# Kernel optimization log

Hardware: AMD Instinct MI355X
Metric: run time of the kernel (lower is better)

Reference implementation:

```python
import jax, jax.numpy as jnp
import numpy as np

B, S, E, N, H = 2, 2048, 2048, 16, 128  # batch, seq, embed, heads, depth


def sine_table(features, length, min_timescale=1.0, max_timescale=10000.0):
    fraction = jnp.arange(0, features, 2, dtype=jnp.float32) / features
    timescale = min_timescale * (max_timescale / min_timescale) ** fraction
    sinusoid_inp = jnp.einsum('i,j->ij', jnp.arange(length, dtype=jnp.float32), 1.0 / timescale,
                              precision=jax.lax.Precision.HIGHEST)
    sinusoid_inp = jnp.concatenate([sinusoid_inp, sinusoid_inp], axis=-1)  # [L, features]
    return jnp.sin(sinusoid_inp), jnp.cos(sinusoid_inp)


def rotate_half(x):
    x1, x2 = jnp.split(x, 2, axis=-1)
    return jnp.concatenate([-x2, x1], axis=-1)


def apply_rotary(q, k, cos, sin):
    # q: [B,S,N,H], k: [B,T,N,H]; cos/sin: [L,H] broadcast over (seq, depth)
    qcos = cos[: q.shape[1]][None, :, None, :]
    qsin = sin[: q.shape[1]][None, :, None, :]
    kcos = cos[: k.shape[1]][None, :, None, :]
    ksin = sin[: k.shape[1]][None, :, None, :]
    return q * qcos + rotate_half(q) * qsin, k * kcos + rotate_half(k) * ksin


def setup_inputs() -> dict:
    key = jax.random.key(0)
    ks = jax.random.split(key, 6)
    scale = 1.0 / np.sqrt(E)
    return {
        'x_q': jax.random.normal(ks[0], (B, S, E), jnp.float32),
        'x_kv': jax.random.normal(ks[1], (B, S, E), jnp.float32),
        'WQ': jax.random.normal(ks[2], (E, N, H), jnp.float32) * scale,
        'WK': jax.random.normal(ks[3], (E, N, H), jnp.float32) * scale,
        'WV': jax.random.normal(ks[4], (E, N, H), jnp.float32) * scale,
        'WO': jax.random.normal(ks[5], (N, H, E), jnp.float32) * scale,
    }


def reference(x_q, x_kv, WQ, WK, WV, WO):
    q = jnp.einsum('bse,enh->bsnh', x_q, WQ)
    k = jnp.einsum('bte,enh->btnh', x_kv, WK)
    v = jnp.einsum('bte,enh->btnh', x_kv, WV)

    sin, cos = sine_table(q.shape[-1], max(q.shape[1], k.shape[1]))
    q, k = apply_rotary(q, k, cos, sin)

    # causal attention bias: [1,1,S,T]
    s_len, t_len = q.shape[1], k.shape[1]
    causal = jnp.arange(s_len)[:, None] >= jnp.arange(t_len)[None, :]
    bias = jnp.where(causal, 0.0, -1e10).astype(jnp.float32)[None, None]

    logits = jnp.einsum('bsnh,btnh->bnst', q, k) / np.sqrt(H) + bias
    probs = jax.nn.softmax(logits, axis=-1)
    a = jnp.einsum('bnst,btnh->bsnh', probs, v)
    o = jnp.einsum('bsnh,nhe->bse', a, WO)
    return o
```

## Files before the change

kernel.cpp:

```cpp
#include <hip/hip_runtime.h>
#include <hip/hip_bf16.h>

typedef __bf16 bf16;
typedef __attribute__((ext_vector_type(8))) __bf16 bf16x8;
typedef __attribute__((ext_vector_type(4))) __bf16 bf16x4;
typedef __attribute__((ext_vector_type(4))) float f32x4;

typedef const __attribute__((address_space(1))) void* gptr_t;
typedef __attribute__((address_space(3))) void* sptr_t;

__device__ __forceinline__ void gload16(const void* g, void* l) {
  __builtin_amdgcn_global_load_lds((gptr_t)g, (sptr_t)l, 16, 0, 0);
}

#define MFMA_BF16(a, b, c) __builtin_amdgcn_mfma_f32_16x16x32_bf16((a), (b), (c), 0, 0, 0)

namespace {
constexpr int kB = 2, kS = 2048, kE = 2048, kN = 16, kH = 128;
constexpr int kBS = kB * kS;
constexpr int kNH = kN * kH;
constexpr float kScale = 0.08838834764831845f;
constexpr float kLog2e = 1.4426950408889634f;
}

__global__ void k_cvt(const float* __restrict__ in, bf16* __restrict__ out) {
  int i = blockIdx.x * 256 + threadIdx.x;
  float4 v = reinterpret_cast<const float4*>(in)[i];
  bf16x4 o = { (bf16)v.x, (bf16)v.y, (bf16)v.z, (bf16)v.w };
  reinterpret_cast<bf16x4*>(out)[i] = o;
}

__global__ void k_tconv(const float* __restrict__ in, bf16* __restrict__ out) {
  __shared__ bf16 tile[64][66];
  int bx = blockIdx.x & 31, by = blockIdx.x >> 5;
  int r0 = by * 64, c0 = bx * 64;
  int t = threadIdx.x;
  int c = t & 63, rb = t >> 6;
#pragma unroll
  for (int j = 0; j < 16; ++j) {
    int r = rb + j * 4;
    tile[r][c] = (bf16)in[(size_t)(r0 + r) * 2048 + c0 + c];
  }
  __syncthreads();
  int rr = t & 63;
#pragma unroll
  for (int j = 0; j < 16; ++j) {
    int cc = rb + j * 4;
    out[(size_t)(c0 + cc) * 2048 + r0 + rr] = tile[rr][cc];
  }
}

__global__ void k_vtrans(const bf16* __restrict__ V, bf16* __restrict__ Vt) {
  __shared__ bf16 tile[64][66];
  int bid = blockIdx.x;
  int bn = bid >> 6;
  int s0 = ((bid >> 1) & 31) * 64;
  int h0 = (bid & 1) * 64;
  size_t base = (size_t)bn * kS * kH;
  int t = threadIdx.x, c = t & 63, rb = t >> 6;
#pragma unroll
  for (int j = 0; j < 16; ++j) {
    int r = rb + j * 4;
    tile[r][c] = V[base + (size_t)(s0 + r) * kH + h0 + c];
  }
  __syncthreads();
#pragma unroll
  for (int j = 0; j < 16; ++j) {
    int hh = rb + j * 4;
    Vt[base + (size_t)(h0 + hh) * kS + s0 + (t & 63)] = tile[t & 63][hh];
  }
}

__global__ void k_rope(bf16* __restrict__ Qd, bf16* __restrict__ Kd) {
  int tid = blockIdx.x * 256 + threadIdx.x;
  int i = tid & 63;
  int s = (tid >> 6) & (kS - 1);
  int bn = tid >> 17;
  size_t base = ((size_t)bn * kS + s) * kH;
  float inv = exp2f(-(float)i * 0.20762050593046457f);
  float ang = (float)s * inv;
  float sn, cs;
  sincosf(ang, &sn, &cs);
  float q1 = (float)Qd[base + i], q2 = (float)Qd[base + i + 64];
  Qd[base + i]      = (bf16)(q1 * cs - q2 * sn);
  Qd[base + i + 64] = (bf16)(q2 * cs + q1 * sn);
  float k1 = (float)Kd[base + i], k2 = (float)Kd[base + i + 64];
  Kd[base + i]      = (bf16)(k1 * cs - k2 * sn);
  Kd[base + i + 64] = (bf16)(k2 * cs + k1 * sn);
}

template <int MODE>
__global__ __launch_bounds__(256, 2) void k_gemm(const bf16* __restrict__ A,
                                                 const bf16* __restrict__ Bt,
                                                 void* __restrict__ Cout) {
  constexpr int Kk = 2048;
  __shared__ __align__(16) bf16 As[128][32];
  __shared__ __align__(16) bf16 Bs[128][32];
  int bid = blockIdx.x;
  int swz = (bid & 7) * 64 + (bid >> 3);
  int mt = swz >> 4, nt = swz & 15;
  int m0 = mt * 128, n0 = nt * 128;
  int t = threadIdx.x, wid = t >> 6, lane = t & 63;
  int l16 = lane & 15, lq = lane >> 4;
  int wr = wid >> 1, wc = wid & 1;
  f32x4 acc[4][4] = {};

  for (int kt = 0; kt < Kk / 32; ++kt) {
    int k0 = kt * 32;
#pragma unroll
    for (int i = 0; i < 2; ++i) {
      int idx = i * 256 + t;
      const bf16* ga = A + (size_t)(m0 + (idx >> 2)) * Kk + k0 + (idx & 3) * 8;
      gload16(ga, (char*)(&As[0][0]) + i * 4096 + wid * 1024);
      const bf16* gb = Bt + (size_t)(n0 + (idx >> 2)) * Kk + k0 + (idx & 3) * 8;
      gload16(gb, (char*)(&Bs[0][0]) + i * 4096 + wid * 1024);
    }
    __syncthreads();
    bf16x8 af[4], bfr[4];
#pragma unroll
    for (int mi = 0; mi < 4; ++mi)
      af[mi] = *(const bf16x8*)&As[wr * 64 + mi * 16 + l16][lq * 8];
#pragma unroll
    for (int ni = 0; ni < 4; ++ni)
      bfr[ni] = *(const bf16x8*)&Bs[wc * 64 + ni * 16 + l16][lq * 8];
#pragma unroll
    for (int mi = 0; mi < 4; ++mi)
#pragma unroll
      for (int ni = 0; ni < 4; ++ni)
        acc[mi][ni] = MFMA_BF16(af[mi], bfr[ni], acc[mi][ni]);
    __syncthreads();
  }

#pragma unroll
  for (int mi = 0; mi < 4; ++mi) {
    int mrow_base = m0 + wr * 64 + mi * 16 + lq * 4;
#pragma unroll
    for (int ni = 0; ni < 4; ++ni) {
      int col = n0 + wc * 64 + ni * 16 + l16;
#pragma unroll
      for (int r = 0; r < 4; ++r) {
        int mrow = mrow_base + r;
        float v = acc[mi][ni][r];
        if (MODE == 0) {
          int b = mrow >> 11, s = mrow & 2047, n = col >> 7, h = col & 127;
          ((bf16*)Cout)[(((size_t)(b * kN + n) * kS + s)) * kH + h] = (bf16)v;
        } else {
          ((float*)Cout)[(size_t)mrow * 2048 + col] = v;
        }
      }
    }
  }
}

__global__ __launch_bounds__(512, 4) void k_attn(const bf16* __restrict__ Q,
                                                 const bf16* __restrict__ Kg,
                                                 const bf16* __restrict__ Vt,
                                                 bf16* __restrict__ AO) {
  __shared__ __align__(16) bf16 Ks[64 * 128];
  __shared__ __align__(16) bf16 Vs[128 * 64];
  __shared__ __align__(16) bf16 Ps[8][16][72];
  int bid = blockIdx.x;
  int half = bid >> 8;
  int bn = (half << 4) | ((bid >> 4) & 15);
  int qt = (bid & 15) ^ (half ? 15 : 0);
  int q0 = qt * 128;
  int t = threadIdx.x, wid = t >> 6, lane = t & 63;
  int l16 = lane & 15, lq = lane >> 4;
  size_t bnSH = (size_t)bn * kS * kH;

  int qrow_a = q0 + wid * 16 + l16;
  bf16x8 qf[4];
#pragma unroll
  for (int ks = 0; ks < 4; ++ks)
    qf[ks] = *(const bf16x8*)(Q + bnSH + (size_t)qrow_a * kH + ks * 32 + lq * 8);

  f32x4 oacc[8] = {};
  float mrun[4], lrun[4];
#pragma unroll
  for (int r = 0; r < 4; ++r) { mrun[r] = -1e30f; lrun[r] = 0.f; }

  int ntiles = (q0 + 128) >> 6;
  for (int kt = 0; kt < ntiles; ++kt) {
    int kv0 = kt * 64;
#pragma unroll
    for (int i = 0; i < 2; ++i) {
      int idx = i * 512 + t;
      {
        int row = idx >> 4, ch = idx & 15;
        int gch = ch ^ (row & 7);
        gload16(Kg + bnSH + (size_t)(kv0 + row) * kH + gch * 8,
                (char*)Ks + i * 8192 + wid * 1024);
      }
      {
        int row = idx >> 3, ch = idx & 7;
        int gch = ch ^ (row & 7);
        gload16(Vt + bnSH + (size_t)row * kS + kv0 + gch * 8,
                (char*)Vs + i * 8192 + wid * 1024);
      }
    }
    __syncthreads();

    f32x4 sacc[4] = {};
#pragma unroll
    for (int ks = 0; ks < 4; ++ks) {
#pragma unroll
      for (int ni = 0; ni < 4; ++ni) {
        int sp = ni * 16 + l16;
        int hb = (ks * 32 + lq * 8) * 2;
        bf16x8 kb = *(const bf16x8*)((const char*)Ks + sp * 256 + (hb ^ ((sp & 7) << 4)));
        sacc[ni] = MFMA_BF16(qf[ks], kb, sacc[ni]);
      }
    }

    bool need_mask = (kv0 + 63) > (q0 + wid * 16);
#pragma unroll
    for (int ni = 0; ni < 4; ++ni) {
      f32x4 v = sacc[ni] * kScale;
      if (need_mask) {
#pragma unroll
        for (int r = 0; r < 4; ++r) {
          int qrow = q0 + wid * 16 + lq * 4 + r;
          int col = kv0 + ni * 16 + l16;
          if (col > qrow) v[r] = -1e30f;
        }
      }
      sacc[ni] = v;
    }

#pragma unroll
    for (int r = 0; r < 4; ++r) {
      float pm = fmaxf(fmaxf(sacc[0][r], sacc[1][r]),
                       fmaxf(sacc[2][r], sacc[3][r]));
      pm = fmaxf(pm, __shfl_xor(pm, 1));
      pm = fmaxf(pm, __shfl_xor(pm, 2));
      pm = fmaxf(pm, __shfl_xor(pm, 4));
      pm = fmaxf(pm, __shfl_xor(pm, 8));
      float mold = mrun[r];
      float mnew = fmaxf(mold, pm);
      float alpha = exp2f((mold - mnew) * kLog2e);
      mrun[r] = mnew;
      float rs = 0.f;
#pragma unroll
      for (int ni = 0; ni < 4; ++ni) {
        float p = exp2f((sacc[ni][r] - mnew) * kLog2e);
        sacc[ni][r] = p;
        rs += p;
      }
      rs += __shfl_xor(rs, 1);
      rs += __shfl_xor(rs, 2);
      rs += __shfl_xor(rs, 4);
      rs += __shfl_xor(rs, 8);
      lrun[r] = lrun[r] * alpha + rs;
#pragma unroll
      for (int nj = 0; nj < 8; ++nj) oacc[nj][r] *= alpha;
    }

#pragma unroll
    for (int ni = 0; ni < 4; ++ni)
#pragma unroll
      for (int r = 0; r < 4; ++r)
        Ps[wid][lq * 4 + r][ni * 16 + l16] = (bf16)sacc[ni][r];

#pragma unroll
    for (int ks = 0; ks < 2; ++ks) {
      bf16x8 pa = *(const bf16x8*)&Ps[wid][l16][ks * 32 + lq * 8];
#pragma unroll
      for (int nj = 0; nj < 8; ++nj) {
        int h = nj * 16 + l16;
        int sb = (ks * 64 + lq * 16) ^ ((h & 7) << 4);
        bf16x8 vb = *(const bf16x8*)((const char*)Vs + h * 128 + sb);
        oacc[nj] = MFMA_BF16(pa, vb, oacc[nj]);
      }
    }
    __syncthreads();
  }

  int b = bn >> 4, n = bn & 15;
#pragma unroll
  for (int r = 0; r < 4; ++r) {
    float inv = 1.0f / lrun[r];
    int qrow = q0 + wid * 16 + lq * 4 + r;
#pragma unroll
    for (int nj = 0; nj < 8; ++nj) {
      float v = oacc[nj][r] * inv;
      AO[(((size_t)b * kS + qrow) * kN + n) * kH + nj * 16 + l16] = (bf16)v;
    }
  }
}

extern "C" void kernel_launch(void* const* d_in, const int* in_sizes, int n_in,
                              void* d_out, int out_size, void* d_ws, size_t ws_size,
                              hipStream_t stream) {
  (void)in_sizes; (void)n_in; (void)out_size; (void)ws_size;
  const float* x_q  = (const float*)d_in[0];
  const float* x_kv = (const float*)d_in[1];
  const float* WQ   = (const float*)d_in[2];
  const float* WK   = (const float*)d_in[3];
  const float* WV   = (const float*)d_in[4];
  const float* WO   = (const float*)d_in[5];
  float* out = (float*)d_out;
  char* w = (char*)d_ws;
  const size_t MB = 1ull << 20;
  bf16* xq  = (bf16*)(w + 0 * MB);
  bf16* xkv = (bf16*)(w + 16 * MB);
  bf16* WqT = (bf16*)(w + 32 * MB);
  bf16* WkT = (bf16*)(w + 40 * MB);
  bf16* WvT = (bf16*)(w + 48 * MB);
  bf16* WoT = (bf16*)(w + 56 * MB);
  bf16* Qb  = (bf16*)(w + 64 * MB);
  bf16* Kb  = (bf16*)(w + 80 * MB);
  bf16* Vb  = (bf16*)(w + 96 * MB);
  bf16* AO  = xq;
  bf16* Vtb = xkv;

  k_cvt<<<8192, 256, 0, stream>>>(x_q, xq);
  k_cvt<<<8192, 256, 0, stream>>>(x_kv, xkv);
  k_tconv<<<1024, 256, 0, stream>>>(WQ, WqT);
  k_tconv<<<1024, 256, 0, stream>>>(WK, WkT);
  k_tconv<<<1024, 256, 0, stream>>>(WV, WvT);
  k_tconv<<<1024, 256, 0, stream>>>(WO, WoT);
  k_gemm<0><<<512, 256, 0, stream>>>(xq,  WqT, Qb);
  k_gemm<0><<<512, 256, 0, stream>>>(xkv, WkT, Kb);
  k_gemm<0><<<512, 256, 0, stream>>>(xkv, WvT, Vb);
  k_rope<<<16384, 256, 0, stream>>>(Qb, Kb);
  k_vtrans<<<2048, 256, 0, stream>>>(Vb, Vtb);
  k_attn<<<512, 512, 0, stream>>>(Qb, Kb, Vtb, AO);
  k_gemm<1><<<512, 256, 0, stream>>>(AO, WoT, out);
}
```

Before: 471.5 us.

## Fuse QKV projections into one 256x256 double-buffered pipelined GEMM kernel

Replaces the 128x128 single-buffered GEMM with a 256x256-tile, 512-thread kernel. It uses double-buffered LDS staged through direct global-to-LDS loads, an XOR-swizzled layout, and raised wave priority around the MFMA bursts. The three Q/K/V projections are merged into one launch over the concatenated weight matrix, with each output routed to Q, K or V by column group. The aim is to cut load stalls, barrier overhead and launch count. The larger tiles leave the output projection with only 128 blocks, which underfills the CUs.

```diff
diff --git a/kernel.cpp b/kernel.cpp
--- a/kernel.cpp
+++ b/kernel.cpp
@@ -15,10 +15,10 @@
 
 #define MFMA_BF16(a, b, c) __builtin_amdgcn_mfma_f32_16x16x32_bf16((a), (b), (c), 0, 0, 0)
 
+#define BAR() do { asm volatile("" ::: "memory"); __builtin_amdgcn_s_barrier(); asm volatile("" ::: "memory"); } while (0)
+
 namespace {
 constexpr int kB = 2, kS = 2048, kE = 2048, kN = 16, kH = 128;
-constexpr int kBS = kB * kS;
-constexpr int kNH = kN * kH;
 constexpr float kScale = 0.08838834764831845f;
 constexpr float kLog2e = 1.4426950408889634f;
 }
@@ -89,63 +89,150 @@
   Kd[base + i + 64] = (bf16)(k2 * cs + k1 * sn);
 }
 
+
+__device__ __forceinline__ void stage_half(const bf16* __restrict__ src, size_t row0,
+                                           int k0, char* slot, int t) {
+#pragma unroll
+  for (int i = 0; i < 2; ++i) {
+    int idx = i * 512 + t;
+    int d = idx * 16;
+    int lb = d ^ (((d >> 9) & 1) << 5);
+    int r = lb >> 7;
+    int kc = (lb & 127) >> 1;
+    gload16(src + (row0 + r) * 2048 + k0 + kc,
+            slot + i * 8192 + (t >> 6) * 1024);
+  }
+}
+
 template <int MODE>
-__global__ __launch_bounds__(256, 2) void k_gemm(const bf16* __restrict__ A,
-                                                 const bf16* __restrict__ Bt,
-                                                 void* __restrict__ Cout) {
-  constexpr int Kk = 2048;
-  __shared__ __align__(16) bf16 As[128][32];
-  __shared__ __align__(16) bf16 Bs[128][32];
+__global__ __launch_bounds__(512, 2) void k_gemm8(const bf16* __restrict__ Aq,
+                                                  const bf16* __restrict__ Akv,
+                                                  const bf16* __restrict__ Bt,
+                                                  void* __restrict__ Cout) {
+  constexpr int NTN = (MODE == 0) ? 24 : 8;
+  constexpr int NT = 32;
+  __shared__ __align__(16) char AsB[2][2][16384];
+  __shared__ __align__(16) char BsB[2][2][16384];
   int bid = blockIdx.x;
-  int swz = (bid & 7) * 64 + (bid >> 3);
-  int mt = swz >> 4, nt = swz & 15;
-  int m0 = mt * 128, n0 = nt * 128;
+  constexpr int nblk = 16 * NTN;
+  int swz = (bid & 7) * (nblk >> 3) + (bid >> 3);
+  int mt = swz / NTN, nt = swz - mt * NTN;
+  size_t m0 = (size_t)mt * 256;
+  int n0 = nt * 256;
+  const bf16* A = (MODE == 0 && nt >= 8) ? Akv : Aq;
   int t = threadIdx.x, wid = t >> 6, lane = t & 63;
   int l16 = lane & 15, lq = lane >> 4;
-  int wr = wid >> 1, wc = wid & 1;
-  f32x4 acc[4][4] = {};
-
-  for (int kt = 0; kt < Kk / 32; ++kt) {
-    int k0 = kt * 32;
-#pragma unroll
-    for (int i = 0; i < 2; ++i) {
-      int idx = i * 256 + t;
-      const bf16* ga = A + (size_t)(m0 + (idx >> 2)) * Kk + k0 + (idx & 3) * 8;
-      gload16(ga, (char*)(&As[0][0]) + i * 4096 + wid * 1024);
-      const bf16* gb = Bt + (size_t)(n0 + (idx >> 2)) * Kk + k0 + (idx & 3) * 8;
-      gload16(gb, (char*)(&Bs[0][0]) + i * 4096 + wid * 1024);
-    }
-    __syncthreads();
-    bf16x8 af[4], bfr[4];
-#pragma unroll
-    for (int mi = 0; mi < 4; ++mi)
-      af[mi] = *(const bf16x8*)&As[wr * 64 + mi * 16 + l16][lq * 8];
-#pragma unroll
-    for (int ni = 0; ni < 4; ++ni)
-      bfr[ni] = *(const bf16x8*)&Bs[wc * 64 + ni * 16 + l16][lq * 8];
-#pragma unroll
-    for (int mi = 0; mi < 4; ++mi)
-#pragma unroll
-      for (int ni = 0; ni < 4; ++ni)
-        acc[mi][ni] = MFMA_BF16(af[mi], bfr[ni], acc[mi][ni]);
-    __syncthreads();
-  }
-
-#pragma unroll
-  for (int mi = 0; mi < 4; ++mi) {
-    int mrow_base = m0 + wr * 64 + mi * 16 + lq * 4;
-#pragma unroll
-    for (int ni = 0; ni < 4; ++ni) {
-      int col = n0 + wc * 64 + ni * 16 + l16;
+  int wr = wid >> 2, wc = wid & 3;
+  int bhalf = wc >> 1;
+  int brow0 = ((wc & 1) << 6) + l16;
+
+  f32x4 acc[8][4] = {};
+  bf16x8 af[4], bf[4];
+
+  stage_half(Bt, (size_t)n0,       0, BsB[0][0], t);
+  stage_half(Bt, (size_t)n0 + 128, 0, BsB[0][1], t);
+  stage_half(A,  m0,               0, AsB[0][0], t);
+  stage_half(A,  m0 + 128,         0, AsB[0][1], t);
+  stage_half(Bt, (size_t)n0,      64, BsB[1][0], t);
+  stage_half(Bt, (size_t)n0 + 128, 64, BsB[1][1], t);
+  asm volatile("s_waitcnt vmcnt(4)" ::: "memory");
+  BAR();
+
+  for (int kt = 0; kt < NT; ++kt) {
+    int buf = kt & 1, nbuf = buf ^ 1;
+#pragma unroll
+    for (int j = 0; j < 4; ++j) {
+      int l = ((j * 16 + l16) << 7) + (lq << 4);
+      af[j] = *(const bf16x8*)(AsB[buf][wr] + (l ^ (((l >> 9) & 1) << 5)));
+    }
+#pragma unroll
+    for (int nf = 0; nf < 4; ++nf) {
+      int l = ((brow0 + nf * 16) << 7) + (lq << 4);
+      bf[nf] = *(const bf16x8*)(BsB[buf][bhalf] + (l ^ (((l >> 9) & 1) << 5)));
+    }
+    if (kt + 1 < NT) stage_half(A, m0, (kt + 1) * 64, AsB[nbuf][0], t);
+    BAR();
+    __builtin_amdgcn_s_setprio(1);
+#pragma unroll
+    for (int j = 0; j < 4; ++j)
+#pragma unroll
+      for (int nf = 0; nf < 4; ++nf)
+        acc[j][nf] = MFMA_BF16(af[j], bf[nf], acc[j][nf]);
+    __builtin_amdgcn_s_setprio(0);
+    BAR();
+#pragma unroll
+    for (int j = 0; j < 4; ++j) {
+      int l = (((j + 4) * 16 + l16) << 7) + (lq << 4);
+      af[j] = *(const bf16x8*)(AsB[buf][wr] + (l ^ (((l >> 9) & 1) << 5)));
+    }
+    if (kt + 1 < NT) stage_half(A, m0 + 128, (kt + 1) * 64, AsB[nbuf][1], t);
+    BAR();
+    __builtin_amdgcn_s_setprio(1);
+#pragma unroll
+    for (int j = 0; j < 4; ++j)
+#pragma unroll
+      for (int nf = 0; nf < 4; ++nf)
+        acc[j + 4][nf] = MFMA_BF16(af[j], bf[nf], acc[j + 4][nf]);
+    __builtin_amdgcn_s_setprio(0);
+    BAR();
+#pragma unroll
+    for (int j = 0; j < 4; ++j) {
+      int l = ((j * 16 + l16) << 7) + 64 + (lq << 4);
+      af[j] = *(const bf16x8*)(AsB[buf][wr] + (l ^ (((l >> 9) & 1) << 5)));
+    }
+#pragma unroll
+    for (int nf = 0; nf < 4; ++nf) {
+      int l = ((brow0 + nf * 16) << 7) + 64 + (lq << 4);
+      bf[nf] = *(const bf16x8*)(BsB[buf][bhalf] + (l ^ (((l >> 9) & 1) << 5)));
+    }
+    BAR();
+    __builtin_amdgcn_s_setprio(1);
+#pragma unroll
+    for (int j = 0; j < 4; ++j)
+#pragma unroll
+      for (int nf = 0; nf < 4; ++nf)
+        acc[j][nf] = MFMA_BF16(af[j], bf[nf], acc[j][nf]);
+    __builtin_amdgcn_s_setprio(0);
+    BAR();
+#pragma unroll
+    for (int j = 0; j < 4; ++j) {
+      int l = (((j + 4) * 16 + l16) << 7) + 64 + (lq << 4);
+      af[j] = *(const bf16x8*)(AsB[buf][wr] + (l ^ (((l >> 9) & 1) << 5)));
+    }
+    if (kt + 2 < NT) {
+      stage_half(Bt, (size_t)n0,       (kt + 2) * 64, BsB[buf][0], t);
+      stage_half(Bt, (size_t)n0 + 128, (kt + 2) * 64, BsB[buf][1], t);
+    }
+    BAR();
+    __builtin_amdgcn_s_setprio(1);
+#pragma unroll
+    for (int j = 0; j < 4; ++j)
+#pragma unroll
+      for (int nf = 0; nf < 4; ++nf)
+        acc[j + 4][nf] = MFMA_BF16(af[j], bf[nf], acc[j + 4][nf]);
+    __builtin_amdgcn_s_setprio(0);
+    if (kt < NT - 2)       asm volatile("s_waitcnt vmcnt(4)" ::: "memory");
+    else if (kt == NT - 2) asm volatile("s_waitcnt vmcnt(0)" ::: "memory");
+    BAR();
+  }
+
+#pragma unroll
+  for (int mf = 0; mf < 8; ++mf) {
+    int rowb = (int)m0 + wr * 128 + mf * 16 + lq * 4;
+#pragma unroll
+    for (int nf = 0; nf < 4; ++nf) {
+      int col = n0 + wc * 64 + nf * 16 + l16;
 #pragma unroll
       for (int r = 0; r < 4; ++r) {
-        int mrow = mrow_base + r;
-        float v = acc[mi][ni][r];
+        float v = acc[mf][nf][r];
+        int mrow = rowb + r;
         if (MODE == 0) {
-          int b = mrow >> 11, s = mrow & 2047, n = col >> 7, h = col & 127;
-          ((bf16*)Cout)[(((size_t)(b * kN + n) * kS + s)) * kH + h] = (bf16)v;
+          int grp = col >> 11, cw = col & 2047;
+          int b = mrow >> 11, s = mrow & 2047, n = cw >> 7, h = cw & 127;
+          ((bf16*)Cout)[(size_t)grp * 8388608 +
+                        (((size_t)(b * 16 + n) * 2048 + s) << 7) + h] = (bf16)v;
         } else {
-          ((float*)Cout)[(size_t)mrow * 2048 + col] = v;
+          ((float*)Cout)[((size_t)mrow << 11) + col] = v;
         }
       }
     }
@@ -319,11 +406,9 @@
   k_tconv<<<1024, 256, 0, stream>>>(WK, WkT);
   k_tconv<<<1024, 256, 0, stream>>>(WV, WvT);
   k_tconv<<<1024, 256, 0, stream>>>(WO, WoT);
-  k_gemm<0><<<512, 256, 0, stream>>>(xq,  WqT, Qb);
-  k_gemm<0><<<512, 256, 0, stream>>>(xkv, WkT, Kb);
-  k_gemm<0><<<512, 256, 0, stream>>>(xkv, WvT, Vb);
+  k_gemm8<0><<<384, 512, 0, stream>>>(xq, xkv, WqT, Qb);
   k_rope<<<16384, 256, 0, stream>>>(Qb, Kb);
   k_vtrans<<<2048, 256, 0, stream>>>(Vb, Vtb);
   k_attn<<<512, 512, 0, stream>>>(Qb, Kb, Vtb, AO);
-  k_gemm<1><<<512, 256, 0, stream>>>(AO, WoT, out);
-}
+  k_gemm8<1><<<128, 512, 0, stream>>>(AO, AO, WoT, out);
+}
```

Result: no change. 474.6 us (+0.7%).
